# Performance work log

Measured on AMD Instinct MI355X. Metric: run time of the kernel, lower is better.

The kernel has to match this reference:

```python
import jax, jax.numpy as jnp
import numpy as np

B, N, P_FEATS = 8, 4096, 3
WIDTH, HEADS, LAYERS, N_LAT = 768, 12, 8, 256
NUM_FREQS = 8
D_HEAD = WIDTH // HEADS
SCALE = 1.0 / np.sqrt(np.sqrt(D_HEAD))  # applied to q and k separately
IN_DIM = 3 * (1 + 2 * NUM_FREQS) + P_FEATS  # 54
EPS = 1e-5


def fourier_embed(pc):
    # pc: [B,N,3] -> [B,N,51] (include_input + sin/cos at freqs 2^0..2^7)
    freqs = (2.0 ** jnp.arange(NUM_FREQS)).astype(pc.dtype)
    ang = pc[..., None] * freqs  # [B,N,3,F]
    ang = ang.reshape(*pc.shape[:-1], 3 * NUM_FREQS)
    return jnp.concatenate([pc, jnp.sin(ang), jnp.cos(ang)], axis=-1)


def layernorm(x, s, b):
    mu = jnp.mean(x, axis=-1, keepdims=True)
    var = jnp.mean(jnp.square(x - mu), axis=-1, keepdims=True)
    return (x - mu) * jax.lax.rsqrt(var + EPS) * s + b


def mh_attn(q, k, v):
    # q: [B,T,H,C], k/v: [B,S,H,C]
    w = jnp.einsum('bthc,bshc->bhts', q * SCALE, k * SCALE)
    w = jax.nn.softmax(w.astype(jnp.float32), axis=-1).astype(q.dtype)
    out = jnp.einsum('bhts,bshc->bthc', w, v)
    return out.reshape(*q.shape[:2], -1)


def setup_inputs() -> dict:
    key = jax.random.key(0)
    ks = iter(jax.random.split(key, 64))
    rn = lambda shape, std=0.02: jax.random.normal(next(ks), shape, jnp.float32) * std
    inp = {
        'pc': jax.random.normal(next(ks), (B, N, 3), jnp.float32),
        'feats': jax.random.uniform(next(ks), (B, N, P_FEATS), jnp.float32),
        'query': rn((N_LAT, WIDTH)),
        'in_W': rn((WIDTH, IN_DIM)), 'in_b': jnp.zeros((WIDTH,)),
        'ca_qkv_W': rn((3 * WIDTH, WIDTH)), 'ca_qkv_b': jnp.zeros((3 * WIDTH,)),
        'ca_proj_W': rn((WIDTH, WIDTH)), 'ca_proj_b': jnp.zeros((WIDTH,)),
        'ln1_s': jnp.ones((LAYERS, WIDTH)), 'ln1_b': jnp.zeros((LAYERS, WIDTH)),
        'qkv_W': rn((LAYERS, 3 * WIDTH, WIDTH)), 'qkv_b': jnp.zeros((LAYERS, 3 * WIDTH)),
        'proj_W': rn((LAYERS, WIDTH, WIDTH)), 'proj_b': jnp.zeros((LAYERS, WIDTH)),
        'ln2_s': jnp.ones((LAYERS, WIDTH)), 'ln2_b': jnp.zeros((LAYERS, WIDTH)),
        'fc_W': rn((LAYERS, 4 * WIDTH, WIDTH)), 'fc_b': jnp.zeros((LAYERS, 4 * WIDTH)),
        'fc2_W': rn((LAYERS, WIDTH, 4 * WIDTH)), 'fc2_b': jnp.zeros((LAYERS, WIDTH)),
    }
    return inp


def _forward(pc, feats, query, in_W, in_b, ca_qkv_W, ca_qkv_b, ca_proj_W, ca_proj_b,
             ln1_s, ln1_b, qkv_W, qkv_b, proj_W, proj_b, ln2_s, ln2_b,
             fc_W, fc_b, fc2_W, fc2_b):
    bs = pc.shape[0]
    data = jnp.concatenate([fourier_embed(pc), feats], axis=-1)  # [B,N,54]
    data = data @ in_W.T + in_b  # [B,N,W]
    q_lat = jnp.broadcast_to(query[None], (bs, N_LAT, WIDTH))

    # --- cross attention (no residual, matching source) ---
    q = (q_lat @ ca_qkv_W.T + ca_qkv_b)[..., :WIDTH]
    kv = data @ ca_qkv_W.T + ca_qkv_b
    k, v = kv[..., WIDTH:2 * WIDTH], kv[..., 2 * WIDTH:]
    q = q.reshape(bs, N_LAT, HEADS, D_HEAD)
    k = k.reshape(bs, N, HEADS, D_HEAD)
    v = v.reshape(bs, N, HEADS, D_HEAD)
    latents = mh_attn(q, k, v) @ ca_proj_W.T + ca_proj_b  # [B,L,W]

    # --- self-attention transformer stack via scan ---
    def block(x, p):
        (l1s, l1b, qW, qb, pW, pb, l2s, l2b, fW, fb, f2W, f2b) = p
        h = layernorm(x, l1s, l1b)
        qkv = (h @ qW.T + qb).reshape(bs, N_LAT, HEADS, 3 * D_HEAD)
        qh, kh, vh = jnp.split(qkv, 3, axis=-1)
        x = x + mh_attn(qh, kh, vh) @ pW.T + pb
        h = layernorm(x, l2s, l2b)
        h = jax.nn.gelu(h @ fW.T + fb, approximate=False) @ f2W.T + f2b
        return x + h, None

    params = (ln1_s, ln1_b, qkv_W, qkv_b, proj_W, proj_b, ln2_s, ln2_b, fc_W, fc_b, fc2_W, fc2_b)
    latents, _ = jax.lax.scan(block, latents, params)
    return latents, pc


def reference(pc, feats, query, in_W, in_b, ca_qkv_W, ca_qkv_b, ca_proj_W, ca_proj_b,
              ln1_s, ln1_b, qkv_W, qkv_b, proj_W, proj_b, ln2_s, ln2_b,
              fc_W, fc_b, fc2_W, fc2_b):
    return _forward(pc, feats, query, in_W, in_b, ca_qkv_W, ca_qkv_b, ca_proj_W, ca_proj_b,
                    ln1_s, ln1_b, qkv_W, qkv_b, proj_W, proj_b, ln2_s, ln2_b,
                    fc_W, fc_b, fc2_W, fc2_b)
```

## Files before the change

kernel.cpp:

```cpp
#include <hip/hip_runtime.h>
#include <stdint.h>

typedef unsigned short u16;
typedef __bf16 bf16x8 __attribute__((ext_vector_type(8)));
typedef float f32x4 __attribute__((ext_vector_type(4)));

#define DEVINL __device__ __forceinline__

DEVINL u16 f2bf(float f) {
  union { float f; unsigned u; } c; c.f = f;
  unsigned u = c.u + 0x7FFFu + ((c.u >> 16) & 1u);
  return (u16)(u >> 16);
}

DEVINL float bf2f(u16 v) {
  union { unsigned u; float f; } c; c.u = (unsigned)v << 16;
  return c.f;
}

DEVINL void gl2lds16(const void* g, void* l) {
  __builtin_amdgcn_global_load_lds(
      (const __attribute__((address_space(1))) unsigned int*)g,
      (__attribute__((address_space(3))) unsigned int*)l, 16, 0, 0);
}

__global__ __launch_bounds__(256) void cvt4_kernel(
    const float* __restrict__ s0, u16* __restrict__ d0, int n0,
    const float* __restrict__ s1, u16* __restrict__ d1, int n1,
    const float* __restrict__ s2, u16* __restrict__ d2, int n2,
    const float* __restrict__ s3, u16* __restrict__ d3, int n3) {
  int i = blockIdx.x * 256 + threadIdx.x;
  const float* s; u16* d;
  if (i < n0) { s = s0; d = d0; }
  else {
    i -= n0;
    if (i < n1) { s = s1; d = d1; }
    else {
      i -= n1;
      if (i < n2) { s = s2; d = d2; }
      else {
        i -= n2;
        if (i >= n3) return;
        s = s3; d = d3;
      }
    }
  }
  float4 v = ((const float4*)s)[i];
  unsigned a = (unsigned)f2bf(v.x) | ((unsigned)f2bf(v.y) << 16);
  unsigned b = (unsigned)f2bf(v.z) | ((unsigned)f2bf(v.w) << 16);
  ((uint2*)d)[i] = make_uint2(a, b);
}

__global__ __launch_bounds__(256) void pad_inw_kernel(const float* __restrict__ src,
                                                      u16* __restrict__ dst) {
  int t = blockIdx.x * 256 + threadIdx.x;
  int r = t >> 6, c = t & 63;
  dst[t] = (c < 54) ? f2bf(src[r * 54 + c]) : (u16)0;
}

__global__ __launch_bounds__(256) void embed_kernel(const float* __restrict__ pc,
                                                    const float* __restrict__ feats,
                                                    u16* __restrict__ emb) {
  int t = blockIdx.x * 256 + threadIdx.x;
  int p = t >> 6, c = t & 63;
  float v = 0.f;
  if (c < 3) {
    v = pc[p * 3 + c];
  } else if (c < 27) {
    int i = c - 3;
    float f = (float)(1 << (i & 7));
    v = sinf(pc[p * 3 + (i >> 3)] * f);
  } else if (c < 51) {
    int i = c - 27;
    float f = (float)(1 << (i & 7));
    v = cosf(pc[p * 3 + (i >> 3)] * f);
  } else if (c < 54) {
    v = feats[p * 3 + (c - 51)];
  }
  emb[t] = f2bf(v);
}

template <int TM, int TN, int WR, int WC>
__global__ __launch_bounds__(256) void gemm_t(
    const u16* __restrict__ A, const u16* __restrict__ Bw,
    const float* __restrict__ bias, const float* __restrict__ resid,
    float* __restrict__ outF, u16* __restrict__ outB,
    int M, int N, int K, int gelu) {
  constexpr int IM = TM / WR / 16;
  constexpr int IN = TN / WC / 16;
  __shared__ u16 As[TM * 32];
  __shared__ u16 Bs[TN * 32];
  const int tid = threadIdx.x;
  const int lane = tid & 63, w = tid >> 6;
  const int l15 = lane & 15, quad = lane >> 4;
  const int mblk = blockIdx.x * TM, nblk = blockIdx.y * TN;
  const int wm = (w % WR) * (TM / WR);
  const int wn = (w / WR) * (TN / WC);

  f32x4 acc[IM][IN];
#pragma unroll
  for (int i = 0; i < IM; i++)
#pragma unroll
    for (int j = 0; j < IN; j++) acc[i][j] = f32x4{0.f, 0.f, 0.f, 0.f};

  for (int k0 = 0; k0 < K; k0 += 32) {
#pragma unroll
    for (int s = tid; s < TM * 4; s += 256) {
      int row = s >> 2, c8 = (s & 3) << 3;
      gl2lds16(A + (size_t)(mblk + row) * K + (k0 + c8), &As[s * 8]);
    }
#pragma unroll
    for (int s = tid; s < TN * 4; s += 256) {
      int row = s >> 2, c8 = (s & 3) << 3;
      gl2lds16(Bw + (size_t)(nblk + row) * K + (k0 + c8), &Bs[s * 8]);
    }
    __syncthreads();
    bf16x8 af[IM], bfr[IN];
#pragma unroll
    for (int i = 0; i < IM; i++)
      af[i] = *(const bf16x8*)&As[(wm + i * 16 + l15) * 32 + quad * 8];
#pragma unroll
    for (int j = 0; j < IN; j++)
      bfr[j] = *(const bf16x8*)&Bs[(wn + j * 16 + l15) * 32 + quad * 8];
#pragma unroll
    for (int i = 0; i < IM; i++)
#pragma unroll
      for (int j = 0; j < IN; j++)
        acc[i][j] = __builtin_amdgcn_mfma_f32_16x16x32_bf16(af[i], bfr[j], acc[i][j], 0, 0, 0);
    __syncthreads();
  }

#pragma unroll
  for (int i = 0; i < IM; i++) {
    int row0 = mblk + wm + i * 16 + quad * 4;
#pragma unroll
    for (int j = 0; j < IN; j++) {
      int col = nblk + wn + j * 16 + l15;
      float bv = bias[col];
#pragma unroll
      for (int r = 0; r < 4; r++) {
        float v = acc[i][j][r] + bv;
        if (gelu) v = 0.5f * v * (1.0f + erff(v * 0.70710678118f));
        size_t idx = (size_t)(row0 + r) * N + col;
        if (resid) v += resid[idx];
        if (outF) outF[idx] = v;
        if (outB) outB[idx] = f2bf(v);
      }
    }
  }
}

__global__ __launch_bounds__(256) void repack_vt_kernel(
    const u16* __restrict__ In, long bstride, int rs, int voff, int hs,
    u16* __restrict__ Vt, int Skv) {
  __shared__ u16 tile[64 * 65];
  int nst = Skv >> 6;
  int bid = blockIdx.x;
  int st = bid % nst;
  int bh = bid / nst;
  int h = bh % 12, b = bh / 12;
  const u16* src = In + (size_t)b * bstride + (size_t)(st * 64) * rs + voff + h * hs;
  int tid = threadIdx.x;
#pragma unroll
  for (int p = 0; p < 2; p++) {
    int slot = tid + p * 256;
    int s = slot >> 3, d8 = (slot & 7) << 3;
    uint4 v = *(const uint4*)(src + (size_t)s * rs + d8);
    u16 tmp[8];
    *(uint4*)tmp = v;
#pragma unroll
    for (int j = 0; j < 8; j++) tile[s * 65 + d8 + j] = tmp[j];
  }
  __syncthreads();
  u16* dst = Vt + ((size_t)(b * 12 + h) * 64) * Skv + st * 64;
#pragma unroll
  for (int p = 0; p < 2; p++) {
    int slot = tid + p * 256;
    int d = slot >> 3, s8 = (slot & 7) << 3;
    u16 tmp[8];
#pragma unroll
    for (int j = 0; j < 8; j++) tmp[j] = tile[(s8 + j) * 65 + d];
    *(uint4*)(dst + (size_t)d * Skv + s8) = *(uint4*)tmp;
  }
}

__global__ __launch_bounds__(256) void flash_kernel(
    const u16* __restrict__ Q, long qb, int qrs, int qhs,
    const u16* __restrict__ Kp, long kb, int krs, int khs,
    const u16* __restrict__ Vt, u16* __restrict__ Out,
    u16* __restrict__ Part, float* __restrict__ Ml,
    int Skv, int nsplit, int kvlen, float scale2) {
  __shared__ u16 Qs[64 * 64];
  __shared__ u16 Ks[64 * 64];
  __shared__ u16 Vs[64 * 64];
  __shared__ u16 Ps[64 * 72];

  const int tid = threadIdx.x;
  const int lane = tid & 63, w = tid >> 6;
  const int l15 = lane & 15, quad = lane >> 4;

  int bid = blockIdx.x;
  int per_bh = nsplit << 2;
  int bh = bid / per_bh;
  int rem = bid - bh * per_bh;
  int split = rem >> 2, qt = rem & 3;
  int h = bh % 12, b = bh / 12;

  const u16* Qbase = Q + (size_t)b * qb + (size_t)(qt * 64) * qrs + h * qhs;
  const u16* Kbase = Kp + (size_t)b * kb + (size_t)h * khs;
  const u16* Vbase = Vt + ((size_t)(b * 12 + h) * 64) * Skv;

#pragma unroll
  for (int p = 0; p < 2; ++p) {
    int slot = tid + p * 256;
    int row = slot >> 3, c = slot & 7;
    int cg = (c - row) & 7;
    gl2lds16(Qbase + (size_t)row * qrs + cg * 8, &Qs[slot * 8]);
  }
  __syncthreads();

  bf16x8 qa[2];
#pragma unroll
  for (int kk = 0; kk < 2; kk++)
    qa[kk] = *(const bf16x8*)&Qs[(w * 16 + l15) * 64 + ((kk * 4 + quad + l15) & 7) * 8];

  f32x4 zero = {0.f, 0.f, 0.f, 0.f};
  f32x4 O[4];
  float m_i[4], l_i[4];
#pragma unroll
  for (int d = 0; d < 4; d++) O[d] = zero;
#pragma unroll
  for (int r = 0; r < 4; r++) { m_i[r] = -1e30f; l_i[r] = 0.f; }

  int kt0 = split * kvlen;
  for (int kt = kt0; kt < kt0 + kvlen; kt += 64) {
#pragma unroll
    for (int p = 0; p < 2; ++p) {
      int slot = tid + p * 256;
      int row = slot >> 3, c = slot & 7;
      int cg = (c - row) & 7;
      gl2lds16(Kbase + (size_t)(kt + row) * krs + cg * 8, &Ks[slot * 8]);
      gl2lds16(Vbase + (size_t)row * Skv + kt + cg * 8, &Vs[slot * 8]);
    }
    __syncthreads();

    f32x4 S[4];
#pragma unroll
    for (int j = 0; j < 4; j++) S[j] = zero;
#pragma unroll
    for (int kk = 0; kk < 2; kk++) {
#pragma unroll
      for (int j = 0; j < 4; j++) {
        bf16x8 kf = *(const bf16x8*)&Ks[(j * 16 + l15) * 64 + ((kk * 4 + quad + l15) & 7) * 8];
        S[j] = __builtin_amdgcn_mfma_f32_16x16x32_bf16(qa[kk], kf, S[j], 0, 0, 0);
      }
    }
    float alpha[4];
#pragma unroll
    for (int r = 0; r < 4; r++) {
      float s0 = S[0][r] * scale2, s1 = S[1][r] * scale2;
      float s2 = S[2][r] * scale2, s3 = S[3][r] * scale2;
      S[0][r] = s0; S[1][r] = s1; S[2][r] = s2; S[3][r] = s3;
      float mx = fmaxf(fmaxf(s0, s1), fmaxf(s2, s3));
#pragma unroll
      for (int msk = 1; msk < 16; msk <<= 1) mx = fmaxf(mx, __shfl_xor(mx, msk, 64));
      float mnew = fmaxf(m_i[r], mx);
      float al = __expf(m_i[r] - mnew);
      m_i[r] = mnew;
      alpha[r] = al;
      float sum = 0.f;
#pragma unroll
      for (int j = 0; j < 4; j++) {
        float pv = __expf(S[j][r] - mnew);
        S[j][r] = pv;
        sum += pv;
      }
#pragma unroll
      for (int msk = 1; msk < 16; msk <<= 1) sum += __shfl_xor(sum, msk, 64);
      l_i[r] = l_i[r] * al + sum;
    }
#pragma unroll
    for (int j = 0; j < 4; j++)
#pragma unroll
      for (int r = 0; r < 4; r++)
        Ps[(w * 16 + quad * 4 + r) * 72 + j * 16 + l15] = f2bf(S[j][r]);
#pragma unroll
    for (int d = 0; d < 4; d++)
#pragma unroll
      for (int r = 0; r < 4; r++) O[d][r] *= alpha[r];
    __asm__ __volatile__("s_waitcnt lgkmcnt(0)" ::: "memory");
#pragma unroll
    for (int kk = 0; kk < 2; kk++) {
      bf16x8 pa = *(const bf16x8*)&Ps[(w * 16 + l15) * 72 + kk * 32 + quad * 8];
#pragma unroll
      for (int d = 0; d < 4; d++) {
        bf16x8 vf = *(const bf16x8*)&Vs[(d * 16 + l15) * 64 + ((kk * 4 + quad + l15) & 7) * 8];
        O[d] = __builtin_amdgcn_mfma_f32_16x16x32_bf16(pa, vf, O[d], 0, 0, 0);
      }
    }
    __syncthreads();
  }

  if (nsplit == 1) {
    u16* Ob = Out + ((size_t)(b * 256 + qt * 64 + w * 16 + quad * 4)) * 768 + h * 64 + l15;
#pragma unroll
    for (int d = 0; d < 4; d++)
#pragma unroll
      for (int r = 0; r < 4; r++) {
        float v = O[d][r] / l_i[r];
        Ob[(size_t)r * 768 + d * 16] = f2bf(v);
      }
  } else {
    u16* Pb = Part + ((size_t)(bh * 4 + qt) * nsplit + split) * 4096;
    int rowb = w * 16 + quad * 4;
#pragma unroll
    for (int d = 0; d < 4; d++)
#pragma unroll
      for (int r = 0; r < 4; r++)
        Pb[(rowb + r) * 64 + d * 16 + l15] = f2bf(O[d][r]);
    if (l15 == 0) {
      float* MlB = Ml + ((size_t)(bh * 4 + qt) * nsplit + split) * 128;
#pragma unroll
      for (int r = 0; r < 4; r++) {
        MlB[rowb + r] = m_i[r];
        MlB[64 + rowb + r] = l_i[r];
      }
    }
  }
}

__global__ __launch_bounds__(256) void freduce_kernel(
    const u16* __restrict__ Part, const float* __restrict__ Ml,
    u16* __restrict__ Out, int nsplit) {
  int bid = blockIdx.x;
  int qt = bid & 3, bh = bid >> 2;
  int h = bh % 12, b = bh / 12;
  int tid = threadIdx.x;
  int r = tid >> 2, dc = tid & 3;
  const float* mlb = Ml + (size_t)(bh * 4 + qt) * nsplit * 128;
  float M = -1e30f;
  for (int s = 0; s < nsplit; s++) M = fmaxf(M, mlb[s * 128 + r]);
  float L = 0.f;
  float accv[16];
#pragma unroll
  for (int i = 0; i < 16; i++) accv[i] = 0.f;
  const u16* pb = Part + (size_t)(bh * 4 + qt) * nsplit * 4096 + r * 64 + dc * 16;
  for (int s = 0; s < nsplit; s++) {
    float wgt = __expf(mlb[s * 128 + r] - M);
    L += wgt * mlb[s * 128 + 64 + r];
#pragma unroll
    for (int i = 0; i < 16; i++) accv[i] += wgt * bf2f(pb[s * 4096 + i]);
  }
  float inv = 1.f / L;
  u16* ob = Out + ((size_t)(b * 256 + qt * 64 + r)) * 768 + h * 64 + dc * 16;
#pragma unroll
  for (int i = 0; i < 16; i++) ob[i] = f2bf(accv[i] * inv);
}

__global__ __launch_bounds__(256) void ln_kernel(const float* __restrict__ X,
                                                 const float* __restrict__ sc,
                                                 const float* __restrict__ bi,
                                                 u16* __restrict__ Hout) {
  int row = blockIdx.x;
  int tid = threadIdx.x;
  const float* x = X + (size_t)row * 768;
  float v0 = x[tid], v1 = x[tid + 256], v2 = x[tid + 512];
  float s = v0 + v1 + v2;
  float q = v0 * v0 + v1 * v1 + v2 * v2;
#pragma unroll
  for (int m = 1; m < 64; m <<= 1) {
    s += __shfl_xor(s, m, 64);
    q += __shfl_xor(q, m, 64);
  }
  __shared__ float rs[4], rq[4];
  if ((tid & 63) == 0) { rs[tid >> 6] = s; rq[tid >> 6] = q; }
  __syncthreads();
  s = rs[0] + rs[1] + rs[2] + rs[3];
  q = rq[0] + rq[1] + rq[2] + rq[3];
  float mu = s * (1.f / 768.f);
  float var = q * (1.f / 768.f) - mu * mu;
  float rstd = rsqrtf(var + 1e-5f);
  u16* ho = Hout + (size_t)row * 768;
  ho[tid]       = f2bf((v0 - mu) * rstd * sc[tid]       + bi[tid]);
  ho[tid + 256] = f2bf((v1 - mu) * rstd * sc[tid + 256] + bi[tid + 256]);
  ho[tid + 512] = f2bf((v2 - mu) * rstd * sc[tid + 512] + bi[tid + 512]);
}

__global__ __launch_bounds__(256) void copy4_kernel(const float* __restrict__ src,
                                                    float* __restrict__ dst, int n4) {
  int i = blockIdx.x * 256 + threadIdx.x;
  if (i < n4) ((float4*)dst)[i] = ((const float4*)src)[i];
}

extern "C" void kernel_launch(void* const* d_in, const int* in_sizes, int n_in,
                              void* d_out, int out_size, void* d_ws, size_t ws_size,
                              hipStream_t stream) {
  const float* pc        = (const float*)d_in[0];
  const float* feats     = (const float*)d_in[1];
  const float* query     = (const float*)d_in[2];
  const float* in_W      = (const float*)d_in[3];
  const float* in_b      = (const float*)d_in[4];
  const float* ca_qkv_W  = (const float*)d_in[5];
  const float* ca_qkv_b  = (const float*)d_in[6];
  const float* ca_proj_W = (const float*)d_in[7];
  const float* ca_proj_b = (const float*)d_in[8];
  const float* ln1_s     = (const float*)d_in[9];
  const float* ln1_b     = (const float*)d_in[10];
  const float* qkv_W     = (const float*)d_in[11];
  const float* qkv_b     = (const float*)d_in[12];
  const float* proj_W    = (const float*)d_in[13];
  const float* proj_b    = (const float*)d_in[14];
  const float* ln2_s     = (const float*)d_in[15];
  const float* ln2_b     = (const float*)d_in[16];
  const float* fc_W      = (const float*)d_in[17];
  const float* fc_b      = (const float*)d_in[18];
  const float* fc2_W     = (const float*)d_in[19];
  const float* fc2_b     = (const float*)d_in[20];

  char* base = (char*)d_ws;
  size_t off = 0;
  auto alloc = [&](size_t bytes) -> char* {
    char* p = base + off;
    off += (bytes + 255) & ~(size_t)255;
    return p;
  };

  u16* Wq      = (u16*)alloc(768 * 64 * 2);
  u16* Wquery  = (u16*)alloc(256 * 768 * 2);
  u16* Wcaqkv  = (u16*)alloc(2304 * 768 * 2);
  u16* Wcaproj = (u16*)alloc(768 * 768 * 2);
  u16* Wlqkv   = (u16*)alloc(2304 * 768 * 2);
  u16* Wlproj  = (u16*)alloc(768 * 768 * 2);
  u16* Wlfc    = (u16*)alloc(3072 * 768 * 2);
  u16* Wlfc2   = (u16*)alloc(768 * 3072 * 2);
  u16* qc      = (u16*)alloc(256 * 768 * 2);
  u16* attn    = (u16*)alloc((size_t)2048 * 768 * 2);
  u16* hbuf    = (u16*)alloc((size_t)2048 * 768 * 2);
  char* uni    = alloc(13369344);
  u16* qkvb    = (u16*)uni;
  u16* VtS     = (u16*)(uni + 9437184);
  u16* fc1     = (u16*)uni;
  u16* Part    = (u16*)uni;
  float* Ml    = (float*)(uni + 12582912);

  size_t fixed_end = off;
  size_t per_b = (size_t)4096 * 64 * 2 + (size_t)4096 * 768 * 2 + (size_t)4096 * 1536 * 2;
  int CB;
  if (fixed_end + 8 * per_b + 4096 <= ws_size) CB = 8;
  else if (fixed_end + 2 * per_b + 4096 <= ws_size) CB = 2;
  else CB = 1;

  u16* emb   = (u16*)alloc((size_t)CB * 4096 * 64 * 2);
  u16* dataB = (u16*)alloc((size_t)CB * 4096 * 768 * 2);
  u16* kvb   = (u16*)alloc((size_t)CB * 4096 * 1536 * 2);
  u16* VtC   = dataB;

  float* latents = (float*)d_out;
  const float scale2 = 0.125f;

  {
    int n0 = 256 * 768 / 4, n1 = 2304 * 768 / 4, n2 = 768 * 768 / 4;
    cvt4_kernel<<<(n0 + n1 + n2 + 255) / 256, 256, 0, stream>>>(
        query, Wquery, n0, ca_qkv_W, Wcaqkv, n1, ca_proj_W, Wcaproj, n2,
        nullptr, nullptr, 0);
  }
  pad_inw_kernel<<<192, 256, 0, stream>>>(in_W, Wq);

  gemm_t<64, 64, 2, 2><<<dim3(4, 12), 256, 0, stream>>>(
      Wquery, Wcaqkv, ca_qkv_b, nullptr, nullptr, qc, 256, 768, 768, 0);

  int nchunk = 8 / CB;
  for (int c = 0; c < nchunk; ++c) {
    int Mc = CB * 4096;
    const float* pc_c = pc + (size_t)c * Mc * 3;
    const float* ft_c = feats + (size_t)c * Mc * 3;
    embed_kernel<<<Mc / 4, 256, 0, stream>>>(pc_c, ft_c, emb);
    gemm_t<128, 128, 2, 2><<<dim3(Mc / 128, 6), 256, 0, stream>>>(
        emb, Wq, in_b, nullptr, nullptr, dataB, Mc, 768, 64, 0);
    gemm_t<128, 128, 2, 2><<<dim3(Mc / 128, 12), 256, 0, stream>>>(
        dataB, Wcaqkv + (size_t)768 * 768, ca_qkv_b + 768, nullptr, nullptr, kvb,
        Mc, 1536, 768, 0);
    repack_vt_kernel<<<CB * 12 * 64, 256, 0, stream>>>(
        kvb, (long)4096 * 1536, 1536, 768, 64, VtC, 4096);
    flash_kernel<<<CB * 12 * 16, 256, 0, stream>>>(
        qc, 0L, 768, 64, kvb, (long)4096 * 1536, 1536, 64, VtC,
        nullptr, Part, Ml, 4096, 4, 1024, scale2);
    freduce_kernel<<<CB * 48, 256, 0, stream>>>(
        Part, Ml, attn + (size_t)c * CB * 256 * 768, 4);
  }
  gemm_t<64, 64, 2, 2><<<dim3(32, 12), 256, 0, stream>>>(
      attn, Wcaproj, ca_proj_b, nullptr, latents, nullptr, 2048, 768, 768, 0);

  for (int l = 0; l < 8; ++l) {
    {
      int n0 = 2304 * 768 / 4, n1 = 768 * 768 / 4, n2 = 3072 * 768 / 4, n3 = n2;
      cvt4_kernel<<<(n0 + n1 + n2 + n3 + 255) / 256, 256, 0, stream>>>(
          qkv_W + (size_t)l * 2304 * 768, Wlqkv, n0,
          proj_W + (size_t)l * 768 * 768, Wlproj, n1,
          fc_W + (size_t)l * 3072 * 768, Wlfc, n2,
          fc2_W + (size_t)l * 768 * 3072, Wlfc2, n3);
    }
    ln_kernel<<<2048, 256, 0, stream>>>(latents, ln1_s + l * 768, ln1_b + l * 768, hbuf);
    gemm_t<64, 128, 1, 4><<<dim3(32, 18), 256, 0, stream>>>(
        hbuf, Wlqkv, qkv_b + l * 2304, nullptr, nullptr, qkvb, 2048, 2304, 768, 0);
    repack_vt_kernel<<<384, 256, 0, stream>>>(qkvb, (long)256 * 2304, 2304, 128, 192, VtS, 256);
    flash_kernel<<<384, 256, 0, stream>>>(
        qkvb, (long)256 * 2304, 2304, 192, qkvb + 64, (long)256 * 2304, 2304, 192,
        VtS, attn, nullptr, nullptr, 256, 1, 256, scale2);
    gemm_t<64, 64, 2, 2><<<dim3(32, 12), 256, 0, stream>>>(
        attn, Wlproj, proj_b + l * 768, latents, latents, nullptr, 2048, 768, 768, 0);
    ln_kernel<<<2048, 256, 0, stream>>>(latents, ln2_s + l * 768, ln2_b + l * 768, hbuf);
    gemm_t<64, 128, 1, 4><<<dim3(32, 24), 256, 0, stream>>>(
        hbuf, Wlfc, fc_b + l * 3072, nullptr, nullptr, fc1, 2048, 3072, 768, 1);
    gemm_t<64, 64, 2, 2><<<dim3(32, 12), 256, 0, stream>>>(
        fc1, Wlfc2, fc2_b + l * 768, latents, latents, nullptr, 2048, 768, 3072, 0);
  }

  copy4_kernel<<<96, 256, 0, stream>>>(pc, (float*)d_out + (size_t)2048 * 768, 98304 / 4);
}
```

Before: 1.573 ms.

## Fuse V-transpose into cross-attn KV GEMM epilogue and vectorize GEMM stores

The cross-attention KV projection GEMM gains a mode where blocks producing V columns write their outputs directly in transposed layout. This removes the separate repack_vt pass and the full KV buffer round-trip. K is now written to its own buffer, and V^T gets a dedicated allocation instead of aliasing dataB. The regular GEMM epilogue swaps the MFMA operand order so each lane holds four consecutive columns, allowing float4 bias/residual loads and vectorized stores. The flash reduce kernel also moves to 16-byte loads and stores. In exchange, the transposed V writes are scattered 8-byte stores, and the workspace now needs room for separate K and V buffers.

```diff
diff --git a/kernel.cpp b/kernel.cpp
--- a/kernel.cpp
+++ b/kernel.cpp
@@ -80,12 +80,13 @@
   emb[t] = f2bf(v);
 }
 
-template <int TM, int TN, int WR, int WC>
+template <int TM, int TN, int WR, int WC, int MODE>
 __global__ __launch_bounds__(256) void gemm_t(
     const u16* __restrict__ A, const u16* __restrict__ Bw,
     const float* __restrict__ bias, const float* __restrict__ resid,
     float* __restrict__ outF, u16* __restrict__ outB,
-    int M, int N, int K, int gelu) {
+    int M, int N, int Nout, int K, int gelu,
+    u16* __restrict__ vt, int vy, int skvt, int bsh) {
   constexpr int IM = TM / WR / 16;
   constexpr int IN = TN / WC / 16;
   __shared__ u16 As[TM * 32];
@@ -103,48 +104,114 @@
 #pragma unroll
     for (int j = 0; j < IN; j++) acc[i][j] = f32x4{0.f, 0.f, 0.f, 0.f};
 
-  for (int k0 = 0; k0 < K; k0 += 32) {
-#pragma unroll
-    for (int s = tid; s < TM * 4; s += 256) {
-      int row = s >> 2, c8 = (s & 3) << 3;
-      gl2lds16(A + (size_t)(mblk + row) * K + (k0 + c8), &As[s * 8]);
-    }
-#pragma unroll
-    for (int s = tid; s < TN * 4; s += 256) {
-      int row = s >> 2, c8 = (s & 3) << 3;
-      gl2lds16(Bw + (size_t)(nblk + row) * K + (k0 + c8), &Bs[s * 8]);
-    }
-    __syncthreads();
-    bf16x8 af[IM], bfr[IN];
-#pragma unroll
-    for (int i = 0; i < IM; i++)
-      af[i] = *(const bf16x8*)&As[(wm + i * 16 + l15) * 32 + quad * 8];
-#pragma unroll
-    for (int j = 0; j < IN; j++)
-      bfr[j] = *(const bf16x8*)&Bs[(wn + j * 16 + l15) * 32 + quad * 8];
-#pragma unroll
-    for (int i = 0; i < IM; i++)
+  const bool tv = (MODE == 1) && ((int)blockIdx.y >= vy);
+
+  if (!tv) {
+    for (int k0 = 0; k0 < K; k0 += 32) {
+#pragma unroll
+      for (int s = tid; s < TM * 4; s += 256) {
+        int row = s >> 2, c8 = (s & 3) << 3;
+        gl2lds16(A + (size_t)(mblk + row) * K + (k0 + c8), &As[s * 8]);
+      }
+#pragma unroll
+      for (int s = tid; s < TN * 4; s += 256) {
+        int row = s >> 2, c8 = (s & 3) << 3;
+        gl2lds16(Bw + (size_t)(nblk + row) * K + (k0 + c8), &Bs[s * 8]);
+      }
+      __syncthreads();
+      bf16x8 af[IM], bfr[IN];
+#pragma unroll
+      for (int i = 0; i < IM; i++)
+        af[i] = *(const bf16x8*)&As[(wm + i * 16 + l15) * 32 + quad * 8];
 #pragma unroll
       for (int j = 0; j < IN; j++)
-        acc[i][j] = __builtin_amdgcn_mfma_f32_16x16x32_bf16(af[i], bfr[j], acc[i][j], 0, 0, 0);
-    __syncthreads();
-  }
-
-#pragma unroll
-  for (int i = 0; i < IM; i++) {
-    int row0 = mblk + wm + i * 16 + quad * 4;
+        bfr[j] = *(const bf16x8*)&Bs[(wn + j * 16 + l15) * 32 + quad * 8];
+#pragma unroll
+      for (int i = 0; i < IM; i++)
+#pragma unroll
+        for (int j = 0; j < IN; j++)
+          acc[i][j] = __builtin_amdgcn_mfma_f32_16x16x32_bf16(bfr[j], af[i], acc[i][j], 0, 0, 0);
+      __syncthreads();
+    }
+#pragma unroll
+    for (int i = 0; i < IM; i++) {
+      int m = mblk + wm + i * 16 + l15;
+#pragma unroll
+      for (int j = 0; j < IN; j++) {
+        int n0 = nblk + wn + j * 16 + quad * 4;
+        float4 bv = *(const float4*)&bias[n0];
+        float v0 = acc[i][j][0] + bv.x;
+        float v1 = acc[i][j][1] + bv.y;
+        float v2 = acc[i][j][2] + bv.z;
+        float v3 = acc[i][j][3] + bv.w;
+        if (gelu) {
+          v0 = 0.5f * v0 * (1.0f + erff(v0 * 0.70710678118f));
+          v1 = 0.5f * v1 * (1.0f + erff(v1 * 0.70710678118f));
+          v2 = 0.5f * v2 * (1.0f + erff(v2 * 0.70710678118f));
+          v3 = 0.5f * v3 * (1.0f + erff(v3 * 0.70710678118f));
+        }
+        size_t idx = (size_t)m * Nout + n0;
+        if (resid) {
+          float4 rv = *(const float4*)&resid[idx];
+          v0 += rv.x; v1 += rv.y; v2 += rv.z; v3 += rv.w;
+        }
+        if (outF) {
+          float4 ov = {v0, v1, v2, v3};
+          *(float4*)&outF[idx] = ov;
+        }
+        if (outB) {
+          unsigned lo = (unsigned)f2bf(v0) | ((unsigned)f2bf(v1) << 16);
+          unsigned hi = (unsigned)f2bf(v2) | ((unsigned)f2bf(v3) << 16);
+          *(uint2*)&outB[idx] = make_uint2(lo, hi);
+        }
+      }
+    }
+  } else {
+    for (int k0 = 0; k0 < K; k0 += 32) {
+#pragma unroll
+      for (int s = tid; s < TM * 4; s += 256) {
+        int row = s >> 2, c8 = (s & 3) << 3;
+        gl2lds16(A + (size_t)(mblk + row) * K + (k0 + c8), &As[s * 8]);
+      }
+#pragma unroll
+      for (int s = tid; s < TN * 4; s += 256) {
+        int row = s >> 2, c8 = (s & 3) << 3;
+        gl2lds16(Bw + (size_t)(nblk + row) * K + (k0 + c8), &Bs[s * 8]);
+      }
+      __syncthreads();
+      bf16x8 af[IM], bfr[IN];
+#pragma unroll
+      for (int i = 0; i < IM; i++)
+        af[i] = *(const bf16x8*)&As[(wm + i * 16 + l15) * 32 + quad * 8];
+#pragma unroll
+      for (int j = 0; j < IN; j++)
+        bfr[j] = *(const bf16x8*)&Bs[(wn + j * 16 + l15) * 32 + quad * 8];
+#pragma unroll
+      for (int i = 0; i < IM; i++)
+#pragma unroll
+        for (int j = 0; j < IN; j++)
+          acc[i][j] = __builtin_amdgcn_mfma_f32_16x16x32_bf16(af[i], bfr[j], acc[i][j], 0, 0, 0);
+      __syncthreads();
+    }
+    int msk = (1 << bsh) - 1;
 #pragma unroll
     for (int j = 0; j < IN; j++) {
-      int col = nblk + wn + j * 16 + l15;
-      float bv = bias[col];
-#pragma unroll
-      for (int r = 0; r < 4; r++) {
-        float v = acc[i][j][r] + bv;
-        if (gelu) v = 0.5f * v * (1.0f + erff(v * 0.70710678118f));
-        size_t idx = (size_t)(row0 + r) * N + col;
-        if (resid) v += resid[idx];
-        if (outF) outF[idx] = v;
-        if (outB) outB[idx] = f2bf(v);
+      int n = nblk + wn + j * 16 + l15;
+      float bv = bias[n];
+      int nv = n - vy * TN;
+#pragma unroll
+      for (int i = 0; i < IM; i++) {
+        int m0 = mblk + wm + i * 16 + quad * 4;
+        int b = m0 >> bsh;
+        int s0 = m0 & msk;
+        float v0 = acc[i][j][0] + bv;
+        float v1 = acc[i][j][1] + bv;
+        float v2 = acc[i][j][2] + bv;
+        float v3 = acc[i][j][3] + bv;
+        unsigned lo = (unsigned)f2bf(v0) | ((unsigned)f2bf(v1) << 16);
+        unsigned hi = (unsigned)f2bf(v2) | ((unsigned)f2bf(v3) << 16);
+        size_t addr = (size_t)(b * 768 + nv) * skvt + s0;
+        *(uint2*)&vt[addr] = make_uint2(lo, hi);
       }
     }
   }
@@ -348,13 +415,19 @@
   for (int s = 0; s < nsplit; s++) {
     float wgt = __expf(mlb[s * 128 + r] - M);
     L += wgt * mlb[s * 128 + 64 + r];
-#pragma unroll
-    for (int i = 0; i < 16; i++) accv[i] += wgt * bf2f(pb[s * 4096 + i]);
+    u16 tmp[16];
+    *(uint4*)tmp = *(const uint4*)(pb + s * 4096);
+    *(uint4*)(tmp + 8) = *(const uint4*)(pb + s * 4096 + 8);
+#pragma unroll
+    for (int i = 0; i < 16; i++) accv[i] += wgt * bf2f(tmp[i]);
   }
   float inv = 1.f / L;
+  u16 ot[16];
+#pragma unroll
+  for (int i = 0; i < 16; i++) ot[i] = f2bf(accv[i] * inv);
   u16* ob = Out + ((size_t)(b * 256 + qt * 64 + r)) * 768 + h * 64 + dc * 16;
-#pragma unroll
-  for (int i = 0; i < 16; i++) ob[i] = f2bf(accv[i] * inv);
+  *(uint4*)ob = *(uint4*)ot;
+  *(uint4*)(ob + 8) = *(uint4*)(ot + 8);
 }
 
 __global__ __launch_bounds__(256) void ln_kernel(const float* __restrict__ X,
@@ -444,7 +517,7 @@
   float* Ml    = (float*)(uni + 12582912);
 
   size_t fixed_end = off;
-  size_t per_b = (size_t)4096 * 64 * 2 + (size_t)4096 * 768 * 2 + (size_t)4096 * 1536 * 2;
+  size_t per_b = (size_t)4096 * 64 * 2 + 3 * ((size_t)4096 * 768 * 2);
   int CB;
   if (fixed_end + 8 * per_b + 4096 <= ws_size) CB = 8;
   else if (fixed_end + 2 * per_b + 4096 <= ws_size) CB = 2;
@@ -452,8 +525,8 @@
 
   u16* emb   = (u16*)alloc((size_t)CB * 4096 * 64 * 2);
   u16* dataB = (u16*)alloc((size_t)CB * 4096 * 768 * 2);
-  u16* kvb   = (u16*)alloc((size_t)CB * 4096 * 1536 * 2);
-  u16* VtC   = dataB;
+  u16* kvbK  = (u16*)alloc((size_t)CB * 4096 * 768 * 2);
+  u16* VtC   = (u16*)alloc((size_t)CB * 4096 * 768 * 2);
 
   float* latents = (float*)d_out;
   const float scale2 = 0.125f;
@@ -466,8 +539,9 @@
   }
   pad_inw_kernel<<<192, 256, 0, stream>>>(in_W, Wq);
 
-  gemm_t<64, 64, 2, 2><<<dim3(4, 12), 256, 0, stream>>>(
-      Wquery, Wcaqkv, ca_qkv_b, nullptr, nullptr, qc, 256, 768, 768, 0);
+  gemm_t<64, 64, 2, 2, 0><<<dim3(4, 12), 256, 0, stream>>>(
+      Wquery, Wcaqkv, ca_qkv_b, nullptr, nullptr, qc,
+      256, 768, 768, 768, 0, nullptr, 0, 0, 0);
 
   int nchunk = 8 / CB;
   for (int c = 0; c < nchunk; ++c) {
@@ -475,21 +549,21 @@
     const float* pc_c = pc + (size_t)c * Mc * 3;
     const float* ft_c = feats + (size_t)c * Mc * 3;
     embed_kernel<<<Mc / 4, 256, 0, stream>>>(pc_c, ft_c, emb);
-    gemm_t<128, 128, 2, 2><<<dim3(Mc / 128, 6), 256, 0, stream>>>(
-        emb, Wq, in_b, nullptr, nullptr, dataB, Mc, 768, 64, 0);
-    gemm_t<128, 128, 2, 2><<<dim3(Mc / 128, 12), 256, 0, stream>>>(
-        dataB, Wcaqkv + (size_t)768 * 768, ca_qkv_b + 768, nullptr, nullptr, kvb,
-        Mc, 1536, 768, 0);
-    repack_vt_kernel<<<CB * 12 * 64, 256, 0, stream>>>(
-        kvb, (long)4096 * 1536, 1536, 768, 64, VtC, 4096);
+    gemm_t<128, 128, 2, 2, 0><<<dim3(Mc / 128, 6), 256, 0, stream>>>(
+        emb, Wq, in_b, nullptr, nullptr, dataB,
+        Mc, 768, 768, 64, 0, nullptr, 0, 0, 0);
+    gemm_t<128, 128, 2, 2, 1><<<dim3(Mc / 128, 12), 256, 0, stream>>>(
+        dataB, Wcaqkv + (size_t)768 * 768, ca_qkv_b + 768, nullptr, nullptr, kvbK,
+        Mc, 1536, 768, 768, 0, VtC, 6, 4096, 12);
     flash_kernel<<<CB * 12 * 16, 256, 0, stream>>>(
-        qc, 0L, 768, 64, kvb, (long)4096 * 1536, 1536, 64, VtC,
+        qc, 0L, 768, 64, kvbK, (long)4096 * 768, 768, 64, VtC,
         nullptr, Part, Ml, 4096, 4, 1024, scale2);
     freduce_kernel<<<CB * 48, 256, 0, stream>>>(
         Part, Ml, attn + (size_t)c * CB * 256 * 768, 4);
   }
-  gemm_t<64, 64, 2, 2><<<dim3(32, 12), 256, 0, stream>>>(
-      attn, Wcaproj, ca_proj_b, nullptr, latents, nullptr, 2048, 768, 768, 0);
+  gemm_t<64, 64, 2, 2, 0><<<dim3(32, 12), 256, 0, stream>>>(
+      attn, Wcaproj, ca_proj_b, nullptr, latents, nullptr,
+      2048, 768, 768, 768, 0, nullptr, 0, 0, 0);
 
   for (int l = 0; l < 8; ++l) {
     {
@@ -501,19 +575,23 @@
           fc2_W + (size_t)l * 768 * 3072, Wlfc2, n3);
     }
     ln_kernel<<<2048, 256, 0, stream>>>(latents, ln1_s + l * 768, ln1_b + l * 768, hbuf);
-    gemm_t<64, 128, 1, 4><<<dim3(32, 18), 256, 0, stream>>>(
-        hbuf, Wlqkv, qkv_b + l * 2304, nullptr, nullptr, qkvb, 2048, 2304, 768, 0);
+    gemm_t<64, 128, 1, 4, 0><<<dim3(32, 18), 256, 0, stream>>>(
+        hbuf, Wlqkv, qkv_b + l * 2304, nullptr, nullptr, qkvb,
+        2048, 2304, 2304, 768, 0, nullptr, 0, 0, 0);
     repack_vt_kernel<<<384, 256, 0, stream>>>(qkvb, (long)256 * 2304, 2304, 128, 192, VtS, 256);
     flash_kernel<<<384, 256, 0, stream>>>(
         qkvb, (long)256 * 2304, 2304, 192, qkvb + 64, (long)256 * 2304, 2304, 192,
         VtS, attn, nullptr, nullptr, 256, 1, 256, scale2);
-    gemm_t<64, 64, 2, 2><<<dim3(32, 12), 256, 0, stream>>>(
-        attn, Wlproj, proj_b + l * 768, latents, latents, nullptr, 2048, 768, 768, 0);
+    gemm_t<64, 64, 2, 2, 0><<<dim3(32, 12), 256, 0, stream>>>(
+        attn, Wlproj, proj_b + l * 768, latents, latents, nullptr,
+        2048, 768, 768, 768, 0, nullptr, 0, 0, 0);
     ln_kernel<<<2048, 256, 0, stream>>>(latents, ln2_s + l * 768, ln2_b + l * 768, hbuf);
-    gemm_t<64, 128, 1, 4><<<dim3(32, 24), 256, 0, stream>>>(
-        hbuf, Wlfc, fc_b + l * 3072, nullptr, nullptr, fc1, 2048, 3072, 768, 1);
-    gemm_t<64, 64, 2, 2><<<dim3(32, 12), 256, 0, stream>>>(
-        fc1, Wlfc2, fc2_b + l * 768, latents, latents, nullptr, 2048, 768, 3072, 0);
+    gemm_t<64, 128, 1, 4, 0><<<dim3(32, 24), 256, 0, stream>>>(
+        hbuf, Wlfc, fc_b + l * 3072, nullptr, nullptr, fc1,
+        2048, 3072, 3072, 768, 1, nullptr, 0, 0, 0);
+    gemm_t<64, 64, 2, 2, 0><<<dim3(32, 12), 256, 0, stream>>>(
+        fc1, Wlfc2, fc2_b + l * 768, latents, latents, nullptr,
+        2048, 768, 768, 3072, 0, nullptr, 0, 0, 0);
   }
 
   copy4_kernel<<<96, 256, 0, stream>>>(pc, (float*)d_out + (size_t)2048 * 768, 98304 / 4);
```

After: 1.495 ms. -5.0%, faster.
